# Kernel optimization log

Hardware: AMD Instinct MI355X
Metric: run time of the kernel (lower is better)

## Reference

```python
import jax, jax.numpy as jnp
import numpy as np

HIDDEN = 4096
N_HEADS = 32
N_KV_HEADS = 8
HEAD_DIM = 128
ROPE_THETA = 1e6
RMS_EPS = 1e-6
SEQ = 2048


def setup_inputs() -> dict:
    key = jax.random.key(0)
    k1, k2, k3 = jax.random.split(key, 3)
    hidden_states = jax.random.normal(k1, (SEQ, HIDDEN), dtype=jnp.float32)
    # fused QKV weight: [hidden, (H + 2*Hkv) * head_dim]
    qkv_out = (N_HEADS + 2 * N_KV_HEADS) * HEAD_DIM
    w_qkv = jax.random.normal(k2, (HIDDEN, qkv_out), dtype=jnp.float32) * (HIDDEN ** -0.5)
    w_o = jax.random.normal(k3, (N_HEADS * HEAD_DIM, HIDDEN), dtype=jnp.float32) * ((N_HEADS * HEAD_DIM) ** -0.5)
    q_norm_w = jnp.ones((HEAD_DIM,), dtype=jnp.float32)
    k_norm_w = jnp.ones((HEAD_DIM,), dtype=jnp.float32)
    # NeoX-style rotary tables [T, head_dim/2]
    pos = jnp.arange(SEQ, dtype=jnp.float32)
    inv_freq = 1.0 / (ROPE_THETA ** (jnp.arange(0, HEAD_DIM, 2, dtype=jnp.float32) / HEAD_DIM))
    freqs = pos[:, None] * inv_freq[None, :]  # [T, d/2]
    cos = jnp.cos(freqs)
    sin = jnp.sin(freqs)
    return {"hidden_states": hidden_states, "cos": cos, "sin": sin,
            "w_qkv": w_qkv, "w_o": w_o, "q_norm_w": q_norm_w, "k_norm_w": k_norm_w}


def _rms_norm(x, w, eps=RMS_EPS):
    # per-head RMSNorm over last dim (head_dim)
    var = jnp.mean(jnp.square(x), axis=-1, keepdims=True)
    return x * jax.lax.rsqrt(var + eps) * w


def _rope(x, cos, sin):
    # NeoX rotate-half: x split into two halves of head_dim
    d2 = x.shape[-1] // 2
    x1, x2 = x[..., :d2], x[..., d2:]
    c = cos[:, None, :]  # [T,1,d/2] broadcast over heads
    s = sin[:, None, :]
    return jnp.concatenate([x1 * c - x2 * s, x2 * c + x1 * s], axis=-1)


def reference(hidden_states, cos, sin, w_qkv, w_o, q_norm_w, k_norm_w):
    T = hidden_states.shape[0]
    H, Hkv, D = N_HEADS, N_KV_HEADS, HEAD_DIM
    G = H // Hkv  # GQA group size
    scale = D ** -0.5

    qkv = hidden_states @ w_qkv  # [T, (H+2Hkv)*D]
    q, k, v = jnp.split(qkv, [H * D, (H + Hkv) * D], axis=1)
    q = q.reshape(T, H, D)
    k = k.reshape(T, Hkv, D)
    v = v.reshape(T, Hkv, D)

    q = _rms_norm(q, q_norm_w)
    k = _rms_norm(k, k_norm_w)
    q = _rope(q, cos, sin)
    k = _rope(k, cos, sin)

    # GQA: group query heads onto shared KV heads
    qg = q.reshape(T, Hkv, G, D)
    scores = jnp.einsum('qhgd,khd->hgqk', qg, k) * scale  # [Hkv,G,T,T]
    causal = jnp.tril(jnp.ones((T, T), dtype=bool))
    scores = jnp.where(causal, scores, jnp.float32(-1e30))
    probs = jax.nn.softmax(scores, axis=-1)
    out = jnp.einsum('hgqk,khd->qhgd', probs, v).reshape(T, H * D)
    return out @ w_o  # [T, hidden]
```

## Files before the change

### kernel.cpp

```cpp
#include <hip/hip_runtime.h>
#include <stdint.h>

#define SEQ   2048
#define HID   4096
#define NQH   32
#define NKVH  8
#define HD    128
#define QKVN  6144

typedef uint16_t u16;
typedef __attribute__((ext_vector_type(8))) short bf16x8;
typedef __attribute__((ext_vector_type(4))) float f32x4;
typedef __attribute__((ext_vector_type(4))) unsigned int u32x4;

static __device__ __forceinline__ float bf2f(u16 h){
  union { float f; unsigned int u; } v; v.u = ((unsigned int)h) << 16; return v.f;
}
static __device__ __forceinline__ u16 f2bf(float f){
  unsigned int u = __float_as_uint(f);
  return (u16)((u + 0x7fffu + ((u >> 16) & 1u)) >> 16);
}
static __device__ __forceinline__ f32x4 mfma16(bf16x8 a, bf16x8 b, f32x4 c){
  return __builtin_amdgcn_mfma_f32_16x16x32_bf16(a, b, c, 0, 0, 0);
}
static __device__ __forceinline__ void gload16(const void* g, void* l){
  __builtin_amdgcn_global_load_lds((const __attribute__((address_space(1))) void*)g,
                                   (__attribute__((address_space(3))) void*)l, 16, 0, 0);
}

__global__ void k_cvt(const float* __restrict__ src, u16* __restrict__ dst, int n4){
  int i = blockIdx.x * blockDim.x + threadIdx.x;
  if (i >= n4) return;
  float4 v = ((const float4*)src)[i];
  uint2 o;
  o.x = (unsigned)f2bf(v.x) | ((unsigned)f2bf(v.y) << 16);
  o.y = (unsigned)f2bf(v.z) | ((unsigned)f2bf(v.w) << 16);
  ((uint2*)dst)[i] = o;
}

__global__ void k_transpose_cvt(const float* __restrict__ src, u16* __restrict__ dst, int K, int N){
  __shared__ float t[32][33];
  int n0 = blockIdx.x * 32, k0 = blockIdx.y * 32;
  int tx = threadIdx.x, ty = threadIdx.y;
#pragma unroll
  for (int i = 0; i < 32; i += 8)
    t[ty + i][tx] = src[(size_t)(k0 + ty + i) * N + n0 + tx];
  __syncthreads();
#pragma unroll
  for (int i = 0; i < 32; i += 8)
    dst[(size_t)(n0 + ty + i) * K + k0 + tx] = f2bf(t[tx][ty + i]);
}

__global__ __launch_bounds__(512) void k_gemm192(const u16* __restrict__ A, const u16* __restrict__ Bt,
                                                 u16* __restrict__ Cv, int M, int N, int K){
  __shared__ __align__(16) u16 Asm[2][256][64];
  __shared__ __align__(16) u16 Bsm[2][192][64];
  const int tid = threadIdx.x, lane = tid & 63, wid = tid >> 6;
  const int wm = wid >> 2, wn = wid & 3;
  const int l16 = lane & 15, lhi = lane >> 4;
  const int rx = l16 & 7;
  const int bid = blockIdx.x;
  const int xcd = bid & 7, jj = bid >> 3;
  const size_t bcol = (size_t)(xcd * 4 + jj % 4) * 192;
  const size_t brow = (size_t)((jj / 4) & 7) * 256;

  const f32x4 vz = {0.f, 0.f, 0.f, 0.f};
  f32x4 acc[8][3];
#pragma unroll
  for (int m = 0; m < 8; m++)
#pragma unroll
    for (int n = 0; n < 3; n++) acc[m][n] = vz;

  const int srow = lane >> 3;
  const int sg   = (lane & 7) ^ srow;
  const u16* Ags = A  + (brow + wid*8 + srow) * (size_t)K + sg*8;
  const u16* Bgs = Bt + (bcol + wid*8 + srow) * (size_t)K + sg*8;
  const int NT = K >> 6, NU = NT >> 1;

#define FRA(buf, mi, kh) (*(const bf16x8*)&Asm[buf][wm*128 + (mi)*16 + l16][(((kh)*4 + lhi) ^ rx) << 3])
#define FRB(buf, ni, kh) (*(const bf16x8*)&Bsm[buf][wn*48 + (ni)*16 + l16][(((kh)*4 + lhi) ^ rx) << 3])
#define STG_A(tile, half) do{ if ((tile) < NT){                                  \
    const size_t ko_ = (size_t)((half)*128) * K + (size_t)(tile) * 64;           \
    gload16(Ags + ko_,                &Asm[(tile)&1][(half)*128 + wid*8][0]);     \
    gload16(Ags + ko_ + (size_t)64*K, &Asm[(tile)&1][(half)*128 + 64 + wid*8][0]); } }while(0)
#define STG_B(tile, r) do{ if ((tile) < NT){                                     \
    const size_t ko_ = (size_t)((r)*64) * K + (size_t)(tile) * 64;               \
    gload16(Bgs + ko_, &Bsm[(tile)&1][(r)*64 + wid*8][0]); } }while(0)

  STG_B(0,0); STG_B(0,1); STG_B(0,2);
  STG_A(0,0); STG_A(0,1);
  STG_B(1,0); STG_B(1,1); STG_B(1,2);
  asm volatile("s_waitcnt vmcnt(3)" ::: "memory");
  __builtin_amdgcn_sched_barrier(0);
  __builtin_amdgcn_s_barrier();

  bf16x8 fA[4][2], fB01[2][2], fB2[2];
  for (int u = 0; u < NU; ++u){
    const int t = 2 * u;
#pragma unroll
    for (int mi = 0; mi < 4; ++mi){ fA[mi][0] = FRA(0, mi, 0); fA[mi][1] = FRA(0, mi, 1); }
#pragma unroll
    for (int ni = 0; ni < 2; ++ni){ fB01[ni][0] = FRB(0, ni, 0); fB01[ni][1] = FRB(0, ni, 1); }
    STG_A(t + 1, 0);
    asm volatile("s_waitcnt lgkmcnt(8)" ::: "memory");
    __builtin_amdgcn_s_barrier();
    asm volatile("s_waitcnt lgkmcnt(0)" ::: "memory");
    __builtin_amdgcn_sched_barrier(0);
    __builtin_amdgcn_s_setprio(1);
#pragma unroll
    for (int kh = 0; kh < 2; ++kh)
#pragma unroll
      for (int mi = 0; mi < 4; ++mi)
#pragma unroll
        for (int ni = 0; ni < 2; ++ni)
          acc[mi][ni] = mfma16(fA[mi][kh], fB01[ni][kh], acc[mi][ni]);
    __builtin_amdgcn_s_setprio(0);
    __builtin_amdgcn_s_barrier();
    fB2[0] = FRB(0, 2, 0); fB2[1] = FRB(0, 2, 1);
    STG_A(t + 1, 1);
    __builtin_amdgcn_s_barrier();
    asm volatile("s_waitcnt lgkmcnt(0)" ::: "memory");
    __builtin_amdgcn_sched_barrier(0);
    __builtin_amdgcn_s_setprio(1);
#pragma unroll
    for (int kh = 0; kh < 2; ++kh)
#pragma unroll
      for (int mi = 0; mi < 4; ++mi)
        acc[mi][2] = mfma16(fA[mi][kh], fB2[kh], acc[mi][2]);
    __builtin_amdgcn_s_setprio(0);
    __builtin_amdgcn_s_barrier();
#pragma unroll
    for (int mi = 0; mi < 4; ++mi){ fA[mi][0] = FRA(0, 4 + mi, 0); fA[mi][1] = FRA(0, 4 + mi, 1); }
    STG_B(t + 2, 0);
    __builtin_amdgcn_s_barrier();
    asm volatile("s_waitcnt lgkmcnt(0)" ::: "memory");
    __builtin_amdgcn_sched_barrier(0);
    __builtin_amdgcn_s_setprio(1);
#pragma unroll
    for (int kh = 0; kh < 2; ++kh)
#pragma unroll
      for (int mi = 0; mi < 4; ++mi)
#pragma unroll
        for (int ni = 0; ni < 2; ++ni)
          acc[4 + mi][ni] = mfma16(fA[mi][kh], fB01[ni][kh], acc[4 + mi][ni]);
    __builtin_amdgcn_s_setprio(0);
    __builtin_amdgcn_s_barrier();
    STG_B(t + 2, 1); STG_B(t + 2, 2);
    __builtin_amdgcn_s_barrier();
    asm volatile("s_waitcnt lgkmcnt(0)" ::: "memory");
    __builtin_amdgcn_sched_barrier(0);
    __builtin_amdgcn_s_setprio(1);
#pragma unroll
    for (int kh = 0; kh < 2; ++kh)
#pragma unroll
      for (int mi = 0; mi < 4; ++mi)
        acc[4 + mi][2] = mfma16(fA[mi][kh], fB2[kh], acc[4 + mi][2]);
    __builtin_amdgcn_s_setprio(0);
    if (u == NU - 1) asm volatile("s_waitcnt vmcnt(0)" ::: "memory");
    else             asm volatile("s_waitcnt vmcnt(3)" ::: "memory");
    __builtin_amdgcn_sched_barrier(0);
    __builtin_amdgcn_s_barrier();
#pragma unroll
    for (int mi = 0; mi < 4; ++mi){ fA[mi][0] = FRA(1, mi, 0); fA[mi][1] = FRA(1, mi, 1); }
#pragma unroll
    for (int ni = 0; ni < 2; ++ni){ fB01[ni][0] = FRB(1, ni, 0); fB01[ni][1] = FRB(1, ni, 1); }
    STG_A(t + 2, 0);
    asm volatile("s_waitcnt lgkmcnt(8)" ::: "memory");
    __builtin_amdgcn_s_barrier();
    asm volatile("s_waitcnt lgkmcnt(0)" ::: "memory");
    __builtin_amdgcn_sched_barrier(0);
    __builtin_amdgcn_s_setprio(1);
#pragma unroll
    for (int kh = 0; kh < 2; ++kh)
#pragma unroll
      for (int mi = 0; mi < 4; ++mi)
#pragma unroll
        for (int ni = 0; ni < 2; ++ni)
          acc[mi][ni] = mfma16(fA[mi][kh], fB01[ni][kh], acc[mi][ni]);
    __builtin_amdgcn_s_setprio(0);
    __builtin_amdgcn_s_barrier();
    fB2[0] = FRB(1, 2, 0); fB2[1] = FRB(1, 2, 1);
    STG_A(t + 2, 1);
    __builtin_amdgcn_s_barrier();
    asm volatile("s_waitcnt lgkmcnt(0)" ::: "memory");
    __builtin_amdgcn_sched_barrier(0);
    __builtin_amdgcn_s_setprio(1);
#pragma unroll
    for (int kh = 0; kh < 2; ++kh)
#pragma unroll
      for (int mi = 0; mi < 4; ++mi)
        acc[mi][2] = mfma16(fA[mi][kh], fB2[kh], acc[mi][2]);
    __builtin_amdgcn_s_setprio(0);
    __builtin_amdgcn_s_barrier();
#pragma unroll
    for (int mi = 0; mi < 4; ++mi){ fA[mi][0] = FRA(1, 4 + mi, 0); fA[mi][1] = FRA(1, 4 + mi, 1); }
    STG_B(t + 3, 0);
    __builtin_amdgcn_s_barrier();
    asm volatile("s_waitcnt lgkmcnt(0)" ::: "memory");
    __builtin_amdgcn_sched_barrier(0);
    __builtin_amdgcn_s_setprio(1);
#pragma unroll
    for (int kh = 0; kh < 2; ++kh)
#pragma unroll
      for (int mi = 0; mi < 4; ++mi)
#pragma unroll
        for (int ni = 0; ni < 2; ++ni)
          acc[4 + mi][ni] = mfma16(fA[mi][kh], fB01[ni][kh], acc[4 + mi][ni]);
    __builtin_amdgcn_s_setprio(0);
    __builtin_amdgcn_s_barrier();
    STG_B(t + 3, 1); STG_B(t + 3, 2);
    __builtin_amdgcn_s_barrier();
    asm volatile("s_waitcnt lgkmcnt(0)" ::: "memory");
    __builtin_amdgcn_sched_barrier(0);
    __builtin_amdgcn_s_setprio(1);
#pragma unroll
    for (int kh = 0; kh < 2; ++kh)
#pragma unroll
      for (int mi = 0; mi < 4; ++mi)
        acc[4 + mi][2] = mfma16(fA[mi][kh], fB2[kh], acc[4 + mi][2]);
    __builtin_amdgcn_s_setprio(0);
    asm volatile("s_waitcnt vmcnt(3)" ::: "memory");
    __builtin_amdgcn_sched_barrier(0);
    __builtin_amdgcn_s_barrier();
  }
#undef FRA
#undef FRB
#undef STG_A
#undef STG_B

#pragma unroll
  for (int mi = 0; mi < 8; mi++)
#pragma unroll
    for (int ni = 0; ni < 3; ni++)
#pragma unroll
      for (int i = 0; i < 4; i++){
        size_t row = brow + wm*128 + mi*16 + lhi*4 + i;
        size_t col = bcol + wn*48 + ni*16 + l16;
        Cv[row * (size_t)N + col] = f2bf(acc[mi][ni][i]);
      }
}

__global__ __launch_bounds__(256) void k_gemm128(const u16* __restrict__ A, const u16* __restrict__ Bt,
                                                 float* __restrict__ Cv, int M, int N, int K){
  __shared__ __align__(16) u16 Asm[2][128][64];
  __shared__ __align__(16) u16 Bsm[2][128][64];
  const int tid = threadIdx.x, lane = tid & 63, wid = tid >> 6;
  const int wm = wid >> 1, wn = wid & 1;
  const int l16 = lane & 15, lhi = lane >> 4;
  const int rx = l16 & 7;
  const int bid = blockIdx.x;
  const int xcd = bid & 7, jj = bid >> 3;
  const size_t bcol = (size_t)(xcd * 4 + (jj & 3)) * 128;
  const size_t brow = (size_t)(jj >> 2) * 128;

  const f32x4 vz = {0.f, 0.f, 0.f, 0.f};
  f32x4 acc[4][4];
#pragma unroll
  for (int m = 0; m < 4; m++)
#pragma unroll
    for (int n = 0; n < 4; n++) acc[m][n] = vz;

  const int srow = lane >> 3;
  const int sg   = (lane & 7) ^ srow;
  const u16* Ags = A  + (brow + wid*8 + srow) * (size_t)K + sg*8;
  const u16* Bgs = Bt + (bcol + wid*8 + srow) * (size_t)K + sg*8;
  const int NT = K >> 6;

#define FRA2(buf, mi, kh) (*(const bf16x8*)&Asm[buf][wm*64 + (mi)*16 + l16][(((kh)*4 + lhi) ^ rx) << 3])
#define FRB2(buf, ni, kh) (*(const bf16x8*)&Bsm[buf][wn*64 + (ni)*16 + l16][(((kh)*4 + lhi) ^ rx) << 3])
#define STG2(tile) do{ if ((tile) < NT){                                          \
    const size_t ko_ = (size_t)(tile) * 64;                                       \
    _Pragma("unroll")                                                             \
    for (int r_ = 0; r_ < 4; ++r_){                                               \
      gload16(Ags + (size_t)(r_*32)*K + ko_, &Asm[(tile)&1][r_*32 + wid*8][0]);   \
      gload16(Bgs + (size_t)(r_*32)*K + ko_, &Bsm[(tile)&1][r_*32 + wid*8][0]);   \
    } } }while(0)

  STG2(0);
  asm volatile("s_waitcnt vmcnt(0)" ::: "memory");
  __builtin_amdgcn_sched_barrier(0);
  __builtin_amdgcn_s_barrier();

  bf16x8 fa[4], fb[4];
  for (int t = 0; t < NT; ++t){
    const int cur = t & 1;
    STG2(t + 1);
#pragma unroll
    for (int mi = 0; mi < 4; ++mi) fa[mi] = FRA2(cur, mi, 0);
#pragma unroll
    for (int ni = 0; ni < 4; ++ni) fb[ni] = FRB2(cur, ni, 0);
    __builtin_amdgcn_s_barrier();
    asm volatile("s_waitcnt lgkmcnt(0)" ::: "memory");
    __builtin_amdgcn_sched_barrier(0);
    __builtin_amdgcn_s_setprio(1);
#pragma unroll
    for (int mi = 0; mi < 4; ++mi)
#pragma unroll
      for (int ni = 0; ni < 4; ++ni)
        acc[mi][ni] = mfma16(fa[mi], fb[ni], acc[mi][ni]);
    __builtin_amdgcn_s_setprio(0);
    __builtin_amdgcn_s_barrier();
#pragma unroll
    for (int mi = 0; mi < 4; ++mi) fa[mi] = FRA2(cur, mi, 1);
#pragma unroll
    for (int ni = 0; ni < 4; ++ni) fb[ni] = FRB2(cur, ni, 1);
    __builtin_amdgcn_s_barrier();
    asm volatile("s_waitcnt lgkmcnt(0)" ::: "memory");
    __builtin_amdgcn_sched_barrier(0);
    __builtin_amdgcn_s_setprio(1);
#pragma unroll
    for (int mi = 0; mi < 4; ++mi)
#pragma unroll
      for (int ni = 0; ni < 4; ++ni)
        acc[mi][ni] = mfma16(fa[mi], fb[ni], acc[mi][ni]);
    __builtin_amdgcn_s_setprio(0);
    asm volatile("s_waitcnt vmcnt(0)" ::: "memory");
    __builtin_amdgcn_sched_barrier(0);
    __builtin_amdgcn_s_barrier();
  }
#undef FRA2
#undef FRB2
#undef STG2

#pragma unroll
  for (int mi = 0; mi < 4; mi++)
#pragma unroll
    for (int ni = 0; ni < 4; ni++)
#pragma unroll
      for (int i = 0; i < 4; i++){
        size_t row = brow + wm*64 + mi*16 + lhi*4 + i;
        size_t col = bcol + wn*64 + ni*16 + l16;
        Cv[row * (size_t)N + col] = acc[mi][ni][i];
      }
}

__global__ __launch_bounds__(256) void k_rmsrope(const u16* __restrict__ qkv, const float* __restrict__ cosp,
                                                 const float* __restrict__ sinp, const float* __restrict__ qw,
                                                 const float* __restrict__ kw, u16* __restrict__ Qr,
                                                 u16* __restrict__ Kr){
  int t = blockIdx.x;
  int lane = threadIdx.x & 63, w = threadIdx.x >> 6;
  int hh = blockIdx.y * 4 + w;
  bool isq = hh < NQH;
  int hl = isq ? hh : hh - NQH;
  const u16* src = qkv + (size_t)t * QKVN + (isq ? hl * HD : NQH * HD + hl * HD);
  unsigned u = *(const unsigned*)(src + 2 * lane);
  float x0 = bf2f((u16)(u & 0xffffu)), x1 = bf2f((u16)(u >> 16));
  float ss = x0 * x0 + x1 * x1;
#pragma unroll
  for (int m = 1; m < 64; m <<= 1) ss += __shfl_xor(ss, m);
  float rs = rsqrtf(ss * (1.f / HD) + 1e-6f);
  const float* wp = isq ? qw : kw;
  float w0 = wp[2 * lane], w1 = wp[2 * lane + 1];
  float xn0 = x0 * rs * w0, xn1 = x1 * rs * w1;
  float p0 = __shfl_xor(xn0, 32), p1 = __shfl_xor(xn1, 32);
  int j0 = (2 * lane) & 63;
  float c0 = cosp[t * 64 + j0], c1 = cosp[t * 64 + j0 + 1];
  float s0 = sinp[t * 64 + j0], s1 = sinp[t * 64 + j0 + 1];
  float o0, o1;
  if (lane < 32){ o0 = xn0 * c0 - p0 * s0; o1 = xn1 * c1 - p1 * s1; }
  else          { o0 = xn0 * c0 + p0 * s0; o1 = xn1 * c1 + p1 * s1; }
  if (isq){ o0 *= 0.08838834764831845f; o1 *= 0.08838834764831845f; }
  u16* dst = isq ? (Qr + ((size_t)hl * SEQ + t) * HD) : (Kr + ((size_t)hl * SEQ + t) * HD);
  *(unsigned*)(dst + 2 * lane) = (unsigned)f2bf(o0) | ((unsigned)f2bf(o1) << 16);
}

__global__ void k_vt(const u16* __restrict__ qkv, u16* __restrict__ VT){
  __shared__ u16 t[32][33];
  int t0 = blockIdx.x * 32, d0 = blockIdx.y * 32, hv = blockIdx.z;
  int tx = threadIdx.x, ty = threadIdx.y;
#pragma unroll
  for (int i = 0; i < 32; i += 8)
    t[ty + i][tx] = qkv[(size_t)(t0 + ty + i) * QKVN + (NQH + NKVH) * HD + hv * HD + d0 + tx];
  __syncthreads();
#pragma unroll
  for (int i = 0; i < 32; i += 8)
    VT[((size_t)hv * HD + d0 + ty + i) * SEQ + t0 + tx] = t[tx][ty + i];
}

__global__ __launch_bounds__(512) void k_attn(const u16* __restrict__ Q, const u16* __restrict__ Kg,
                                              const u16* __restrict__ VTg, u16* __restrict__ AO){
  __shared__ __align__(16) u16 Ksm[2][128][128];
  __shared__ __align__(16) u16 Vsm[128][128];
  __shared__ __align__(16) u16 Psm[8][16][136];
  int tid = threadIdx.x, lane = tid & 63, wid = tid >> 6;
  int l16 = lane & 15, lhi = lane >> 4;
  int bid = blockIdx.x;
  int kvg = bid & 7, rr = bid >> 3;
  int J = 15 - (rr >> 2);
  int hq = kvg * 4 + (rr & 3);
  int qb = J * 128;
  const u16* Kh = Kg  + (size_t)kvg * SEQ * HD;
  const u16* Vh = VTg + (size_t)kvg * HD * SEQ;
  const u16* Qh = Q   + (size_t)hq * SEQ * HD;

  bf16x8 qf[4];
#pragma unroll
  for (int ks = 0; ks < 4; ks++)
    qf[ks] = *(const bf16x8*)(Qh + (size_t)(qb + wid*16 + l16) * HD + ks*32 + lhi*8);

  const f32x4 vz = {0.f, 0.f, 0.f, 0.f};
  f32x4 o[8];
  float mrow[4], lrow[4];
#pragma unroll
  for (int n = 0; n < 8; n++) o[n] = vz;
#pragma unroll
  for (int i = 0; i < 4; i++){ mrow[i] = -1e30f; lrow[i] = 0.f; }

  int rsub = lane >> 4, g = lane & 15;
  const u16 *Ks0, *Ks1, *Ks2, *Ks3, *Vs0, *Vs1, *Vs2, *Vs3;
  {
    int r0 = wid*16 + 0*4 + rsub, r1 = wid*16 + 1*4 + rsub;
    int r2 = wid*16 + 2*4 + rsub, r3 = wid*16 + 3*4 + rsub;
    Ks0 = Kh + (size_t)r0 * HD + ((g ^ (r0 & 7)) << 3);
    Ks1 = Kh + (size_t)r1 * HD + ((g ^ (r1 & 7)) << 3);
    Ks2 = Kh + (size_t)r2 * HD + ((g ^ (r2 & 7)) << 3);
    Ks3 = Kh + (size_t)r3 * HD + ((g ^ (r3 & 7)) << 3);
    Vs0 = Vh + (size_t)r0 * SEQ + ((g ^ (r0 & 7)) << 3);
    Vs1 = Vh + (size_t)r1 * SEQ + ((g ^ (r1 & 7)) << 3);
    Vs2 = Vh + (size_t)r2 * SEQ + ((g ^ (r2 & 7)) << 3);
    Vs3 = Vh + (size_t)r3 * SEQ + ((g ^ (r3 & 7)) << 3);
  }

  gload16(Ks0, &Ksm[0][wid*16 +  0][0]);
  gload16(Ks1, &Ksm[0][wid*16 +  4][0]);
  gload16(Ks2, &Ksm[0][wid*16 +  8][0]);
  gload16(Ks3, &Ksm[0][wid*16 + 12][0]);
  asm volatile("s_waitcnt vmcnt(0)" ::: "memory");
  __builtin_amdgcn_sched_barrier(0);
  __builtin_amdgcn_s_barrier();

  int ntr = J + 1;
  int wrow0 = qb + wid*16;
  for (int t = 0; t < ntr; t++){
    int cur = t & 1, nxt = cur ^ 1;
    int kt0 = t << 7;
    bool pf = (t + 1 < ntr);
    gload16(Vs0 + kt0, &Vsm[wid*16 +  0][0]);
    gload16(Vs1 + kt0, &Vsm[wid*16 +  4][0]);
    gload16(Vs2 + kt0, &Vsm[wid*16 +  8][0]);
    gload16(Vs3 + kt0, &Vsm[wid*16 + 12][0]);
    if (pf){
      size_t ko = (size_t)(kt0 + 128) * HD;
      gload16(Ks0 + ko, &Ksm[nxt][wid*16 +  0][0]);
      gload16(Ks1 + ko, &Ksm[nxt][wid*16 +  4][0]);
      gload16(Ks2 + ko, &Ksm[nxt][wid*16 +  8][0]);
      gload16(Ks3 + ko, &Ksm[nxt][wid*16 + 12][0]);
    }
    f32x4 s[8];
#pragma unroll
    for (int n = 0; n < 8; n++) s[n] = vz;
    const u16* kbase = &Ksm[cur][0][0];
    __builtin_amdgcn_s_setprio(1);
#pragma unroll
    for (int n = 0; n < 8; n++){
      int row = n*16 + l16, rxk = row & 7;
#pragma unroll
      for (int ks = 0; ks < 4; ks++){
        bf16x8 kf = *(const bf16x8*)(kbase + row*128 + (((ks*4 + lhi) ^ rxk) << 3));
        s[n] = mfma16(qf[ks], kf, s[n]);
      }
    }
    __builtin_amdgcn_s_setprio(0);
    if (kt0 + 127 > wrow0){
#pragma unroll
      for (int n = 0; n < 8; n++)
#pragma unroll
        for (int i = 0; i < 4; i++)
          if (kt0 + n*16 + l16 > wrow0 + lhi*4 + i) s[n][i] = -1e30f;
    }
#pragma unroll
    for (int i = 0; i < 4; i++){
      float tm = fmaxf(fmaxf(fmaxf(s[0][i], s[1][i]), fmaxf(s[2][i], s[3][i])),
                       fmaxf(fmaxf(s[4][i], s[5][i]), fmaxf(s[6][i], s[7][i])));
      tm = fmaxf(tm, __shfl_xor(tm, 1));
      tm = fmaxf(tm, __shfl_xor(tm, 2));
      tm = fmaxf(tm, __shfl_xor(tm, 4));
      tm = fmaxf(tm, __shfl_xor(tm, 8));
      float nm = fmaxf(mrow[i], tm);
      float sc = __expf(mrow[i] - nm);
      mrow[i] = nm;
      float rsum = 0.f;
#pragma unroll
      for (int n = 0; n < 8; n++){
        float p = __expf(s[n][i] - nm);
        s[n][i] = p;
        rsum += p;
      }
      rsum += __shfl_xor(rsum, 1);
      rsum += __shfl_xor(rsum, 2);
      rsum += __shfl_xor(rsum, 4);
      rsum += __shfl_xor(rsum, 8);
      lrow[i] = lrow[i] * sc + rsum;
#pragma unroll
      for (int n = 0; n < 8; n++) o[n][i] *= sc;
    }
#pragma unroll
    for (int n = 0; n < 8; n++)
#pragma unroll
      for (int i = 0; i < 4; i++)
        Psm[wid][lhi*4 + i][n*16 + l16] = f2bf(s[n][i]);
    if (pf) asm volatile("s_waitcnt vmcnt(4)" ::: "memory");
    else    asm volatile("s_waitcnt vmcnt(0)" ::: "memory");
    __builtin_amdgcn_sched_barrier(0);
    __builtin_amdgcn_s_barrier();
    __builtin_amdgcn_sched_barrier(0);
    __builtin_amdgcn_s_setprio(1);
#pragma unroll
    for (int ksv = 0; ksv < 4; ksv++){
      bf16x8 pa = *(const bf16x8*)&Psm[wid][l16][ksv*32 + lhi*8];
#pragma unroll
      for (int n = 0; n < 8; n++){
        int row = n*16 + l16;
        bf16x8 vb = *(const bf16x8*)(&Vsm[0][0] + row*128 + (((ksv*4 + lhi) ^ (row & 7)) << 3));
        o[n] = mfma16(pa, vb, o[n]);
      }
    }
    __builtin_amdgcn_s_setprio(0);
    asm volatile("s_waitcnt vmcnt(0)" ::: "memory");
    __builtin_amdgcn_sched_barrier(0);
    __builtin_amdgcn_s_barrier();
  }
  float inv[4];
#pragma unroll
  for (int i = 0; i < 4; i++) inv[i] = 1.f / lrow[i];
#pragma unroll
  for (int n = 0; n < 8; n++)
#pragma unroll
    for (int i = 0; i < 4; i++){
      int trow = wrow0 + lhi*4 + i;
      AO[(size_t)trow * HID + hq * HD + n*16 + l16] = f2bf(o[n][i] * inv[i]);
    }
}

extern "C" void kernel_launch(void* const* d_in, const int* in_sizes, int n_in,
                              void* d_out, int out_size, void* d_ws, size_t ws_size,
                              hipStream_t stream){
  const float* hs   = (const float*)d_in[0];
  const float* cosp = (const float*)d_in[1];
  const float* sinp = (const float*)d_in[2];
  const float* wqkv = (const float*)d_in[3];
  const float* wo   = (const float*)d_in[4];
  const float* qw   = (const float*)d_in[5];
  const float* kw   = (const float*)d_in[6];
  float* out = (float*)d_out;
  char* ws = (char*)d_ws;
  u16* XB    = (u16*)(ws + 0);
  u16* WQKVT = (u16*)(ws + 16777216);
  u16* WOT   = (u16*)(ws + 0);
  u16* QKV   = (u16*)(ws + 67108864);
  u16* QR    = (u16*)(ws + 92274688);
  u16* KR    = (u16*)(ws + 109051904);
  u16* VTB   = (u16*)(ws + 113246208);
  u16* AOB   = (u16*)(ws + 117440512);

  k_cvt<<<(SEQ * HID / 4 + 255) / 256, 256, 0, stream>>>(hs, XB, SEQ * HID / 4);
  k_transpose_cvt<<<dim3(QKVN / 32, HID / 32), dim3(32, 8), 0, stream>>>(wqkv, WQKVT, HID, QKVN);
  k_gemm192<<<256, 512, 0, stream>>>(XB, WQKVT, QKV, SEQ, QKVN, HID);
  k_transpose_cvt<<<dim3(HID / 32, HID / 32), dim3(32, 8), 0, stream>>>(wo, WOT, HID, HID);
  k_rmsrope<<<dim3(SEQ, 10), 256, 0, stream>>>(QKV, cosp, sinp, qw, kw, QR, KR);
  k_vt<<<dim3(SEQ / 32, HD / 32, NKVH), dim3(32, 8), 0, stream>>>(QKV, VTB);
  k_attn<<<512, 512, 0, stream>>>(QR, KR, VTB, AOB);
  k_gemm128<<<512, 256, 0, stream>>>(AOB, WOT, out, SEQ, HID, HID);
}
```

Measured before the change: 331.9 us.

## Pair causal query blocks per attention workgroup to balance work and reuse K/V

Each attention workgroup now handles two 128-row query blocks, JA and 15-JA, from the same head. The K/V tiles streamed for the longer block are reused by the shorter block while it is still active. This halves the grid to 256 workgroups, evens out causal load imbalance, and cuts K/V global traffic per query. The cost is doubled accumulator registers (two sets of O, m and l), which may lower occupancy or cause spills, and fewer workgroups to fill the CUs.

Result: slower. 370.2 us (+11.5%).

```diff
diff --git a/kernel.cpp b/kernel.cpp
--- a/kernel.cpp
+++ b/kernel.cpp
@@ -387,25 +387,28 @@
   int l16 = lane & 15, lhi = lane >> 4;
   int bid = blockIdx.x;
   int kvg = bid & 7, rr = bid >> 3;
-  int J = 15 - (rr >> 2);
+  int JA = rr >> 2;
+  int JB = 15 - JA;
   int hq = kvg * 4 + (rr & 3);
-  int qb = J * 128;
+  int qbA = JA * 128, qbB = JB * 128;
   const u16* Kh = Kg  + (size_t)kvg * SEQ * HD;
   const u16* Vh = VTg + (size_t)kvg * HD * SEQ;
   const u16* Qh = Q   + (size_t)hq * SEQ * HD;
 
-  bf16x8 qf[4];
-#pragma unroll
-  for (int ks = 0; ks < 4; ks++)
-    qf[ks] = *(const bf16x8*)(Qh + (size_t)(qb + wid*16 + l16) * HD + ks*32 + lhi*8);
+  bf16x8 qfA[4], qfB[4];
+#pragma unroll
+  for (int ks = 0; ks < 4; ks++){
+    qfA[ks] = *(const bf16x8*)(Qh + (size_t)(qbA + wid*16 + l16) * HD + ks*32 + lhi*8);
+    qfB[ks] = *(const bf16x8*)(Qh + (size_t)(qbB + wid*16 + l16) * HD + ks*32 + lhi*8);
+  }
 
   const f32x4 vz = {0.f, 0.f, 0.f, 0.f};
-  f32x4 o[8];
-  float mrow[4], lrow[4];
-#pragma unroll
-  for (int n = 0; n < 8; n++) o[n] = vz;
-#pragma unroll
-  for (int i = 0; i < 4; i++){ mrow[i] = -1e30f; lrow[i] = 0.f; }
+  f32x4 oA[8], oB[8];
+  float mA[4], lA[4], mB[4], lB[4];
+#pragma unroll
+  for (int n = 0; n < 8; n++){ oA[n] = vz; oB[n] = vz; }
+#pragma unroll
+  for (int i = 0; i < 4; i++){ mA[i] = -1e30f; lA[i] = 0.f; mB[i] = -1e30f; lB[i] = 0.f; }
 
   int rsub = lane >> 4, g = lane & 15;
   const u16 *Ks0, *Ks1, *Ks2, *Ks3, *Vs0, *Vs1, *Vs2, *Vs3;
@@ -430,12 +433,13 @@
   __builtin_amdgcn_sched_barrier(0);
   __builtin_amdgcn_s_barrier();
 
-  int ntr = J + 1;
-  int wrow0 = qb + wid*16;
+  int ntr = JB + 1;
+  int wrA = qbA + wid*16, wrB = qbB + wid*16;
   for (int t = 0; t < ntr; t++){
     int cur = t & 1, nxt = cur ^ 1;
     int kt0 = t << 7;
     bool pf = (t + 1 < ntr);
+    bool actA = (t <= JA);
     gload16(Vs0 + kt0, &Vsm[wid*16 +  0][0]);
     gload16(Vs1 + kt0, &Vsm[wid*16 +  4][0]);
     gload16(Vs2 + kt0, &Vsm[wid*16 +  8][0]);
@@ -447,10 +451,10 @@
       gload16(Ks2 + ko, &Ksm[nxt][wid*16 +  8][0]);
       gload16(Ks3 + ko, &Ksm[nxt][wid*16 + 12][0]);
     }
-    f32x4 s[8];
-#pragma unroll
-    for (int n = 0; n < 8; n++) s[n] = vz;
     const u16* kbase = &Ksm[cur][0][0];
+    f32x4 sB[8];
+#pragma unroll
+    for (int n = 0; n < 8; n++) sB[n] = vz;
     __builtin_amdgcn_s_setprio(1);
 #pragma unroll
     for (int n = 0; n < 8; n++){
@@ -458,48 +462,97 @@
 #pragma unroll
       for (int ks = 0; ks < 4; ks++){
         bf16x8 kf = *(const bf16x8*)(kbase + row*128 + (((ks*4 + lhi) ^ rxk) << 3));
-        s[n] = mfma16(qf[ks], kf, s[n]);
-      }
-    }
-    __builtin_amdgcn_s_setprio(0);
-    if (kt0 + 127 > wrow0){
+        sB[n] = mfma16(qfB[ks], kf, sB[n]);
+      }
+    }
+    __builtin_amdgcn_s_setprio(0);
+    if (kt0 + 127 > wrB){
 #pragma unroll
       for (int n = 0; n < 8; n++)
 #pragma unroll
         for (int i = 0; i < 4; i++)
-          if (kt0 + n*16 + l16 > wrow0 + lhi*4 + i) s[n][i] = -1e30f;
+          if (kt0 + n*16 + l16 > wrB + lhi*4 + i) sB[n][i] = -1e30f;
     }
 #pragma unroll
     for (int i = 0; i < 4; i++){
-      float tm = fmaxf(fmaxf(fmaxf(s[0][i], s[1][i]), fmaxf(s[2][i], s[3][i])),
-                       fmaxf(fmaxf(s[4][i], s[5][i]), fmaxf(s[6][i], s[7][i])));
+      float tm = fmaxf(fmaxf(fmaxf(sB[0][i], sB[1][i]), fmaxf(sB[2][i], sB[3][i])),
+                       fmaxf(fmaxf(sB[4][i], sB[5][i]), fmaxf(sB[6][i], sB[7][i])));
       tm = fmaxf(tm, __shfl_xor(tm, 1));
       tm = fmaxf(tm, __shfl_xor(tm, 2));
       tm = fmaxf(tm, __shfl_xor(tm, 4));
       tm = fmaxf(tm, __shfl_xor(tm, 8));
-      float nm = fmaxf(mrow[i], tm);
-      float sc = __expf(mrow[i] - nm);
-      mrow[i] = nm;
+      float nm = fmaxf(mB[i], tm);
+      float sc = __expf(mB[i] - nm);
+      mB[i] = nm;
       float rsum = 0.f;
 #pragma unroll
       for (int n = 0; n < 8; n++){
-        float p = __expf(s[n][i] - nm);
-        s[n][i] = p;
+        float p = __expf(sB[n][i] - nm);
+        sB[n][i] = p;
         rsum += p;
       }
       rsum += __shfl_xor(rsum, 1);
       rsum += __shfl_xor(rsum, 2);
       rsum += __shfl_xor(rsum, 4);
       rsum += __shfl_xor(rsum, 8);
-      lrow[i] = lrow[i] * sc + rsum;
-#pragma unroll
-      for (int n = 0; n < 8; n++) o[n][i] *= sc;
+      lB[i] = lB[i] * sc + rsum;
+#pragma unroll
+      for (int n = 0; n < 8; n++) oB[n][i] *= sc;
+    }
+    f32x4 sA[8];
+    if (actA){
+#pragma unroll
+      for (int n = 0; n < 8; n++) sA[n] = vz;
+      __builtin_amdgcn_s_setprio(1);
+#pragma unroll
+      for (int n = 0; n < 8; n++){
+        int row = n*16 + l16, rxk = row & 7;
+#pragma unroll
+        for (int ks = 0; ks < 4; ks++){
+          bf16x8 kf = *(const bf16x8*)(kbase + row*128 + (((ks*4 + lhi) ^ rxk) << 3));
+          sA[n] = mfma16(qfA[ks], kf, sA[n]);
+        }
+      }
+      __builtin_amdgcn_s_setprio(0);
+      if (kt0 + 127 > wrA){
+#pragma unroll
+        for (int n = 0; n < 8; n++)
+#pragma unroll
+          for (int i = 0; i < 4; i++)
+            if (kt0 + n*16 + l16 > wrA + lhi*4 + i) sA[n][i] = -1e30f;
+      }
+#pragma unroll
+      for (int i = 0; i < 4; i++){
+        float tm = fmaxf(fmaxf(fmaxf(sA[0][i], sA[1][i]), fmaxf(sA[2][i], sA[3][i])),
+                         fmaxf(fmaxf(sA[4][i], sA[5][i]), fmaxf(sA[6][i], sA[7][i])));
+        tm = fmaxf(tm, __shfl_xor(tm, 1));
+        tm = fmaxf(tm, __shfl_xor(tm, 2));
+        tm = fmaxf(tm, __shfl_xor(tm, 4));
+        tm = fmaxf(tm, __shfl_xor(tm, 8));
+        float nm = fmaxf(mA[i], tm);
+        float sc = __expf(mA[i] - nm);
+        mA[i] = nm;
+        float rsum = 0.f;
+#pragma unroll
+        for (int n = 0; n < 8; n++){
+          float p = __expf(sA[n][i] - nm);
+          sA[n][i] = p;
+          rsum += p;
+        }
+        rsum += __shfl_xor(rsum, 1);
+        rsum += __shfl_xor(rsum, 2);
+        rsum += __shfl_xor(rsum, 4);
+        rsum += __shfl_xor(rsum, 8);
+        lA[i] = lA[i] * sc + rsum;
+#pragma unroll
+        for (int n = 0; n < 8; n++) oA[n][i] *= sc;
+      }
     }
 #pragma unroll
     for (int n = 0; n < 8; n++)
 #pragma unroll
       for (int i = 0; i < 4; i++)
-        Psm[wid][lhi*4 + i][n*16 + l16] = f2bf(s[n][i]);
+        Psm[wid][lhi*4 + i][n*16 + l16] = f2bf(sB[n][i]);
     if (pf) asm volatile("s_waitcnt vmcnt(4)" ::: "memory");
     else    asm volatile("s_waitcnt vmcnt(0)" ::: "memory");
     __builtin_amdgcn_sched_barrier(0);
@@ -513,23 +566,44 @@
       for (int n = 0; n < 8; n++){
         int row = n*16 + l16;
         bf16x8 vb = *(const bf16x8*)(&Vsm[0][0] + row*128 + (((ksv*4 + lhi) ^ (row & 7)) << 3));
-        o[n] = mfma16(pa, vb, o[n]);
-      }
-    }
-    __builtin_amdgcn_s_setprio(0);
+        oB[n] = mfma16(pa, vb, oB[n]);
+      }
+    }
+    __builtin_amdgcn_s_setprio(0);
+    if (actA){
+      __builtin_amdgcn_sched_barrier(0);
+#pragma unroll
+      for (int n = 0; n < 8; n++)
+#pragma unroll
+        for (int i = 0; i < 4; i++)
+          Psm[wid][lhi*4 + i][n*16 + l16] = f2bf(sA[n][i]);
+      __builtin_amdgcn_s_setprio(1);
+#pragma unroll
+      for (int ksv = 0; ksv < 4; ksv++){
+        bf16x8 pa = *(const bf16x8*)&Psm[wid][l16][ksv*32 + lhi*8];
+#pragma unroll
+        for (int n = 0; n < 8; n++){
+          int row = n*16 + l16;
+          bf16x8 vb = *(const bf16x8*)(&Vsm[0][0] + row*128 + (((ksv*4 + lhi) ^ (row & 7)) << 3));
+          oA[n] = mfma16(pa, vb, oA[n]);
+        }
+      }
+      __builtin_amdgcn_s_setprio(0);
+    }
     asm volatile("s_waitcnt vmcnt(0)" ::: "memory");
     __builtin_amdgcn_sched_barrier(0);
     __builtin_amdgcn_s_barrier();
   }
-  float inv[4];
-#pragma unroll
-  for (int i = 0; i < 4; i++) inv[i] = 1.f / lrow[i];
+  float invA[4], invB[4];
+#pragma unroll
+  for (int i = 0; i < 4; i++){ invA[i] = 1.f / lA[i]; invB[i] = 1.f / lB[i]; }
 #pragma unroll
   for (int n = 0; n < 8; n++)
 #pragma unroll
     for (int i = 0; i < 4; i++){
-      int trow = wrow0 + lhi*4 + i;
-      AO[(size_t)trow * HID + hq * HD + n*16 + l16] = f2bf(o[n][i] * inv[i]);
+      int trA = wrA + lhi*4 + i, trB = wrB + lhi*4 + i;
+      AO[(size_t)trA * HID + hq * HD + n*16 + l16] = f2bf(oA[n][i] * invA[i]);
+      AO[(size_t)trB * HID + hq * HD + n*16 + l16] = f2bf(oB[n][i] * invB[i]);
     }
 }
 
@@ -560,6 +634,6 @@
   k_transpose_cvt<<<dim3(HID / 32, HID / 32), dim3(32, 8), 0, stream>>>(wo, WOT, HID, HID);
   k_rmsrope<<<dim3(SEQ, 10), 256, 0, stream>>>(QKV, cosp, sinp, qw, kw, QR, KR);
   k_vt<<<dim3(SEQ / 32, HD / 32, NKVH), dim3(32, 8), 0, stream>>>(QKV, VTB);
-  k_attn<<<512, 512, 0, stream>>>(QR, KR, VTB, AOB);
+  k_attn<<<256, 512, 0, stream>>>(QR, KR, VTB, AOB);
   k_gemm128<<<512, 256, 0, stream>>>(AOB, WOT, out, SEQ, HID, HID);
 }
```
